# Performance work log

Hardware: AMD Instinct MI355X
Metric: run time of the kernel (lower is better)

Reference implementation:

```python
import jax, jax.numpy as jnp
import numpy as np

NDIR = 6      # build_tree.num_directions()
IDIM = 256
ODIM = 512
B, L, NCH = 8, 4096, 8192


def setup_inputs() -> dict:
    key = jax.random.key(0)
    ks = jax.random.split(key, 9)
    last = jax.random.normal(ks[0], (B, NCH, IDIM), dtype=jnp.float32)
    child_l = jax.random.randint(ks[1], (L,), 0, NCH, dtype=jnp.int32)
    child_r = jax.random.randint(ks[2], (L,), 0, NCH, dtype=jnp.int32)
    vec = jax.random.randint(ks[3], (B, L), 0, NCH, dtype=jnp.int32)
    drev = jax.random.randint(ks[4], (NCH,), 0, 2, dtype=jnp.int32)
    dmap = jax.random.randint(ks[5], (NCH,), 0, NDIR, dtype=jnp.int32)
    # merge FC params: ndir independent Linear(2*idim -> odim) + PReLU(init=relu_weight)
    scale = 1.0 / np.sqrt(2 * IDIM)
    W_merge = jax.random.uniform(ks[6], (NDIR, ODIM, 2 * IDIM), jnp.float32, -scale, scale)
    b_merge = jax.random.uniform(ks[7], (NDIR, ODIM), jnp.float32, -scale, scale)
    alpha_merge = jnp.full((NDIR,), 0.005, dtype=jnp.float32)  # PReLU weight (relu_weight)
    return {"last": last, "W_merge": W_merge, "b_merge": b_merge,
            "alpha_merge": alpha_merge, "child_l": child_l, "child_r": child_r,
            "vec": vec, "drev": drev, "dmap": dmap}


def reference(last, W_merge, b_merge, alpha_merge, child_l, child_r, vec, drev, dmap):
    # child gathers: [B, L, idim]
    lch = last[:, child_l]
    rch = last[:, child_r]
    # per-element direction-reverse blending
    d = drev[vec][:, :, None].astype(last.dtype)          # [B, L, 1]
    a = lch * (1.0 - d) + rch * d
    b = rch * (1.0 - d) + lch * d
    ans = jnp.concatenate([a, b], axis=-1)                # [B, L, 2*idim]
    # routed merge: compute all ndir linears, then select per element (ndir is small)
    y_all = jnp.einsum('bli,doi->bldo', ans, W_merge) + b_merge   # [B, L, ndir, odim]
    dir_idx = dmap[vec]                                   # [B, L] in [0, ndir)
    y = jnp.take_along_axis(y_all, dir_idx[:, :, None, None], axis=2)[:, :, 0]  # [B, L, odim]
    alpha = alpha_merge[dir_idx][:, :, None]              # per-element PReLU slope
    return jnp.where(y > 0, y, alpha * y)
```

## Files before the change

### kernel.cpp

```cpp
#include <hip/hip_runtime.h>
#include <hip/hip_bf16.h>

#define BB 8
#define LL 4096
#define NCH 8192
#define IDIM 256
#define KDIM 512
#define ODIM 512
#define NDIR 6
#define TOT (BB * LL)

typedef short short8 __attribute__((ext_vector_type(8)));
typedef float floatx4 __attribute__((ext_vector_type(4)));

#define IDX_OFF (64 + 2 * TOT)
#define PACKA_OFF_INTS (64 + (2 + NDIR) * TOT)
#define PACKA_ELEMS ((long long)NDIR * TOT * KDIM)
#define W_ELEMS (NDIR * ODIM * KDIM)
#define N_W8 (W_ELEMS / 8)

__device__ inline void async_copy16(const void* g, void* l) {
  __builtin_amdgcn_global_load_lds(
      (const __attribute__((address_space(1))) void*)g,
      (__attribute__((address_space(3))) void*)l, 16, 0, 0);
}

__global__ __launch_bounds__(256) void scatter_kernel(
    const int* __restrict__ vec, const int* __restrict__ child_l,
    const int* __restrict__ child_r, const int* __restrict__ drev,
    const int* __restrict__ dmap, int* __restrict__ ws) {
  __shared__ int lcnt[8];
  __shared__ int gbase[8];
  int tid = threadIdx.x;
  if (tid < 8) lcnt[tid] = 0;
  __syncthreads();

  int lin = blockIdx.x * 256 + tid;
  int l = lin & (LL - 1);
  int v = vec[lin];
  int dir = dmap[v] & 7;
  int sw = drev[v];
  int cl = child_l[l];
  int cr = child_r[l];
  int r0 = sw ? cr : cl;
  int r1 = sw ? cl : cr;
  int pos = atomicAdd(&lcnt[dir], 1);
  __syncthreads();
  if (tid < 8) gbase[tid] = lcnt[tid] ? atomicAdd(&ws[tid], lcnt[tid]) : 0;
  __syncthreads();
  int slot = dir * TOT + gbase[dir] + pos;
  ws[64 + lin] = slot;
  ws[64 + TOT + lin] = r0 | (r1 << 16);
}

__global__ __launch_bounds__(256) void pack_kernel(
    const float* __restrict__ last, const float* __restrict__ W,
    int* __restrict__ ws) {
  __hip_bfloat16* packedA = (__hip_bfloat16*)(ws + PACKA_OFF_INTS);
  __hip_bfloat16* W_bf = packedA + PACKA_ELEMS;
  int bid = blockIdx.x;
  if (bid < TOT / 4) {
    int tid = threadIdx.x;
    int t = bid * 4 + (tid >> 6);
    int L = tid & 63;
    int slot = ws[64 + t];
    int rr = ws[64 + TOT + t];
    int b = t >> 12;
    int r = (L < 32) ? (rr & (NCH - 1)) : ((rr >> 16) & (NCH - 1));
    const floatx4* src =
        (const floatx4*)(last + (long long)(b * NCH + r) * IDIM) + (L & 31) * 2;
    floatx4 x0 = src[0];
    floatx4 x1 = src[1];
    union { short8 v; __hip_bfloat16 h[8]; } u;
    u.h[0] = __float2bfloat16(x0[0]); u.h[1] = __float2bfloat16(x0[1]);
    u.h[2] = __float2bfloat16(x0[2]); u.h[3] = __float2bfloat16(x0[3]);
    u.h[4] = __float2bfloat16(x1[0]); u.h[5] = __float2bfloat16(x1[1]);
    u.h[6] = __float2bfloat16(x1[2]); u.h[7] = __float2bfloat16(x1[3]);
    ((short8*)(packedA + (long long)slot * KDIM + (L >> 5) * IDIM))[L & 31] = u.v;
    if (L == 0) ws[IDX_OFF + slot] = t;
  } else {
    int gid = (bid - TOT / 4) * 256 + threadIdx.x;
    const floatx4* s = (const floatx4*)W;
    floatx4 a = s[2 * gid];
    floatx4 b = s[2 * gid + 1];
    union { short8 v; __hip_bfloat16 h[8]; } u;
    u.h[0] = __float2bfloat16(a[0]); u.h[1] = __float2bfloat16(a[1]);
    u.h[2] = __float2bfloat16(a[2]); u.h[3] = __float2bfloat16(a[3]);
    u.h[4] = __float2bfloat16(b[0]); u.h[5] = __float2bfloat16(b[1]);
    u.h[6] = __float2bfloat16(b[2]); u.h[7] = __float2bfloat16(b[3]);
    ((short8*)W_bf)[gid] = u.v;
  }
}

__global__ __launch_bounds__(256) void gemm_kernel(
    const float* __restrict__ bias, const float* __restrict__ alpha_m,
    const int* __restrict__ ws, float* __restrict__ out) {
  __shared__ __hip_bfloat16 Als[2][128 * 32];
  __shared__ __hip_bfloat16 Bls[2][128 * 32];

  const int mt = blockIdx.y;
  const int nt = blockIdx.x;
  int d = -1, count = 0, m_base = 0;
  {
    int tb = 0;
    for (int dd = 0; dd < NDIR; ++dd) {
      int c = ws[dd];
      int ntile = (c + 127) >> 7;
      if (mt < tb + ntile) { d = dd; count = c; m_base = (mt - tb) * 128; break; }
      tb += ntile;
    }
  }
  if (d < 0) return;

  const __hip_bfloat16* packedA = (const __hip_bfloat16*)(ws + PACKA_OFF_INTS);
  const __hip_bfloat16* W_bf = packedA + PACKA_ELEMS;

  const int tid = threadIdx.x;
  const int wave = __builtin_amdgcn_readfirstlane(tid >> 6);
  const int lane = tid & 63;
  const int lane15 = lane & 15;
  const int quad = lane >> 4;
  const int wm = wave >> 1;
  const int wn = wave & 1;
  const int n_blk = nt * 128;

  const __hip_bfloat16* pa[2];
  const __hip_bfloat16* pb[2];
  int ldsbase[2];
  {
    int f = (lane >> 3) & 3;
    int su = ((lane & 3) ^ f) * 8;
#pragma unroll
    for (int i = 0; i < 2; ++i) {
      int sr = wave * 32 + i * 16 + (lane >> 2);
      ldsbase[i] = (wave * 32 + i * 16) * 32;
      int lr = m_base + sr;
      if (lr >= count) lr = count - 1;
      pa[i] = packedA + (long long)(d * TOT + lr) * KDIM + su;
      pb[i] = W_bf + (long long)(d * ODIM + n_blk + sr) * KDIM + su;
    }
  }

  floatx4 acc[4][4] = {};
  const int xq = (lane15 >> 1) & 3;
  const int xcol = (quad ^ xq) * 8;

#pragma unroll
  for (int i = 0; i < 2; ++i) {
    async_copy16(pa[i], &Als[0][ldsbase[i]]);
    async_copy16(pb[i], &Bls[0][ldsbase[i]]);
  }

#pragma unroll
  for (int kt = 0; kt < 16; ++kt) {
    __syncthreads();
    if (kt < 15) {
      const int nb = (kt + 1) & 1;
      const int ko = (kt + 1) * 32;
#pragma unroll
      for (int i = 0; i < 2; ++i) {
        async_copy16(pa[i] + ko, &Als[nb][ldsbase[i]]);
        async_copy16(pb[i] + ko, &Bls[nb][ldsbase[i]]);
      }
    }
    const int c = kt & 1;
    short8 a[4], b[4];
#pragma unroll
    for (int i = 0; i < 4; ++i)
      a[i] = *(const short8*)&Als[c][(wm * 64 + i * 16 + lane15) * 32 + xcol];
#pragma unroll
    for (int j = 0; j < 4; ++j)
      b[j] = *(const short8*)&Bls[c][(wn * 64 + j * 16 + lane15) * 32 + xcol];
#pragma unroll
    for (int i = 0; i < 4; ++i)
#pragma unroll
      for (int j = 0; j < 4; ++j)
        acc[i][j] = __builtin_amdgcn_mfma_f32_16x16x32_bf16(a[i], b[j], acc[i][j], 0, 0, 0);
  }

  const float alpha = alpha_m[d];
  float bj[4];
#pragma unroll
  for (int j = 0; j < 4; ++j)
    bj[j] = bias[d * ODIM + n_blk + wn * 64 + j * 16 + lane15];

#pragma unroll
  for (int i = 0; i < 4; ++i) {
#pragma unroll
    for (int reg = 0; reg < 4; ++reg) {
      int row_id = m_base + wm * 64 + i * 16 + quad * 4 + reg;
      if (row_id >= count) continue;
      int t = ws[IDX_OFF + d * TOT + row_id] & (TOT - 1);
      float* orow = out + (long long)t * ODIM + n_blk + wn * 64;
#pragma unroll
      for (int j = 0; j < 4; ++j) {
        float y = acc[i][j][reg] + bj[j];
        y = y > 0.f ? y : alpha * y;
        orow[j * 16 + lane15] = y;
      }
    }
  }
}

extern "C" void kernel_launch(void* const* d_in, const int* in_sizes, int n_in,
                              void* d_out, int out_size, void* d_ws, size_t ws_size,
                              hipStream_t stream) {
  const float* last = (const float*)d_in[0];
  const float* W = (const float*)d_in[1];
  const float* bias = (const float*)d_in[2];
  const float* alpha = (const float*)d_in[3];
  const int* child_l = (const int*)d_in[4];
  const int* child_r = (const int*)d_in[5];
  const int* vec = (const int*)d_in[6];
  const int* drev = (const int*)d_in[7];
  const int* dmap = (const int*)d_in[8];

  int* ws = (int*)d_ws;

  hipMemsetAsync(ws, 0, 64 * sizeof(int), stream);
  scatter_kernel<<<TOT / 256, 256, 0, stream>>>(vec, child_l, child_r, drev, dmap, ws);
  pack_kernel<<<TOT / 4 + N_W8 / 256, 256, 0, stream>>>(last, W, ws);
  dim3 grid(ODIM / 128, TOT / 128 + NDIR, 1);
  gemm_kernel<<<grid, 256, 0, stream>>>(bias, alpha, ws, (float*)d_out);
}
```

Before: 176.6 us.

## Gather child rows directly in GEMM instead of materializing packed A

Drops the packed, direction-sorted bf16 A buffer. The prep kernel now converts all of `last` and W to bf16, and the GEMM gathers the two child rows per output row straight from bf16 `last` through per-slot index and row tables written by the scatter kernel. The M tile shrinks from 128 to 64 rows so the launch has more blocks. This avoids writing and re-reading the large packed intermediate, at the cost of converting the whole `last` tensor, including rows that are never used, and of scattered gather loads inside the GEMM.

```diff
diff --git a/kernel.cpp b/kernel.cpp
--- a/kernel.cpp
+++ b/kernel.cpp
@@ -9,20 +9,36 @@
 #define ODIM 512
 #define NDIR 6
 #define TOT (BB * LL)
+#define MT 64
 
 typedef short short8 __attribute__((ext_vector_type(8)));
 typedef float floatx4 __attribute__((ext_vector_type(4)));
 
-#define IDX_OFF (64 + 2 * TOT)
-#define PACKA_OFF_INTS (64 + (2 + NDIR) * TOT)
-#define PACKA_ELEMS ((long long)NDIR * TOT * KDIM)
+#define IDX_OFF 64
+#define ROWS_OFF (64 + NDIR * TOT)
+#define LASTBF_OFF (64 + 2 * NDIR * TOT)
+#define LAST_ELEMS (BB * NCH * IDIM)
 #define W_ELEMS (NDIR * ODIM * KDIM)
+#define N_LAST8 (LAST_ELEMS / 8)
 #define N_W8 (W_ELEMS / 8)
 
 __device__ inline void async_copy16(const void* g, void* l) {
   __builtin_amdgcn_global_load_lds(
       (const __attribute__((address_space(1))) void*)g,
       (__attribute__((address_space(3))) void*)l, 16, 0, 0);
+}
+
+__device__ inline void cvt8(const float* __restrict__ src,
+                            __hip_bfloat16* __restrict__ dst, int i) {
+  const floatx4* s = (const floatx4*)src;
+  floatx4 a = s[2 * i];
+  floatx4 b = s[2 * i + 1];
+  union { short8 v; __hip_bfloat16 h[8]; } u;
+  u.h[0] = __float2bfloat16(a[0]); u.h[1] = __float2bfloat16(a[1]);
+  u.h[2] = __float2bfloat16(a[2]); u.h[3] = __float2bfloat16(a[3]);
+  u.h[4] = __float2bfloat16(b[0]); u.h[5] = __float2bfloat16(b[1]);
+  u.h[6] = __float2bfloat16(b[2]); u.h[7] = __float2bfloat16(b[3]);
+  ((short8*)dst)[i] = u.v;
 }
 
 __global__ __launch_bounds__(256) void scatter_kernel(
@@ -35,9 +51,9 @@
   if (tid < 8) lcnt[tid] = 0;
   __syncthreads();
 
-  int lin = blockIdx.x * 256 + tid;
-  int l = lin & (LL - 1);
-  int v = vec[lin];
+  int t = blockIdx.x * 256 + tid;
+  int l = t & (LL - 1);
+  int v = vec[t];
   int dir = dmap[v] & 7;
   int sw = drev[v];
   int cl = child_l[l];
@@ -49,53 +65,24 @@
   if (tid < 8) gbase[tid] = lcnt[tid] ? atomicAdd(&ws[tid], lcnt[tid]) : 0;
   __syncthreads();
   int slot = dir * TOT + gbase[dir] + pos;
-  ws[64 + lin] = slot;
-  ws[64 + TOT + lin] = r0 | (r1 << 16);
-}
-
-__global__ __launch_bounds__(256) void pack_kernel(
+  ws[IDX_OFF + slot] = t;
+  ws[ROWS_OFF + slot] = r0 | (r1 << 16);
+}
+
+__global__ __launch_bounds__(256) void prep_kernel(
     const float* __restrict__ last, const float* __restrict__ W,
     int* __restrict__ ws) {
-  __hip_bfloat16* packedA = (__hip_bfloat16*)(ws + PACKA_OFF_INTS);
-  __hip_bfloat16* W_bf = packedA + PACKA_ELEMS;
-  int bid = blockIdx.x;
-  if (bid < TOT / 4) {
-    int tid = threadIdx.x;
-    int t = bid * 4 + (tid >> 6);
-    int L = tid & 63;
-    int slot = ws[64 + t];
-    int rr = ws[64 + TOT + t];
-    int b = t >> 12;
-    int r = (L < 32) ? (rr & (NCH - 1)) : ((rr >> 16) & (NCH - 1));
-    const floatx4* src =
-        (const floatx4*)(last + (long long)(b * NCH + r) * IDIM) + (L & 31) * 2;
-    floatx4 x0 = src[0];
-    floatx4 x1 = src[1];
-    union { short8 v; __hip_bfloat16 h[8]; } u;
-    u.h[0] = __float2bfloat16(x0[0]); u.h[1] = __float2bfloat16(x0[1]);
-    u.h[2] = __float2bfloat16(x0[2]); u.h[3] = __float2bfloat16(x0[3]);
-    u.h[4] = __float2bfloat16(x1[0]); u.h[5] = __float2bfloat16(x1[1]);
-    u.h[6] = __float2bfloat16(x1[2]); u.h[7] = __float2bfloat16(x1[3]);
-    ((short8*)(packedA + (long long)slot * KDIM + (L >> 5) * IDIM))[L & 31] = u.v;
-    if (L == 0) ws[IDX_OFF + slot] = t;
-  } else {
-    int gid = (bid - TOT / 4) * 256 + threadIdx.x;
-    const floatx4* s = (const floatx4*)W;
-    floatx4 a = s[2 * gid];
-    floatx4 b = s[2 * gid + 1];
-    union { short8 v; __hip_bfloat16 h[8]; } u;
-    u.h[0] = __float2bfloat16(a[0]); u.h[1] = __float2bfloat16(a[1]);
-    u.h[2] = __float2bfloat16(a[2]); u.h[3] = __float2bfloat16(a[3]);
-    u.h[4] = __float2bfloat16(b[0]); u.h[5] = __float2bfloat16(b[1]);
-    u.h[6] = __float2bfloat16(b[2]); u.h[7] = __float2bfloat16(b[3]);
-    ((short8*)W_bf)[gid] = u.v;
-  }
+  __hip_bfloat16* last_bf = (__hip_bfloat16*)(ws + LASTBF_OFF);
+  __hip_bfloat16* W_bf = last_bf + LAST_ELEMS;
+  int gid = blockIdx.x * 256 + threadIdx.x;
+  if (gid < N_LAST8) cvt8(last, last_bf, gid);
+  else cvt8(W, W_bf, gid - N_LAST8);
 }
 
 __global__ __launch_bounds__(256) void gemm_kernel(
     const float* __restrict__ bias, const float* __restrict__ alpha_m,
     const int* __restrict__ ws, float* __restrict__ out) {
-  __shared__ __hip_bfloat16 Als[2][128 * 32];
+  __shared__ __hip_bfloat16 Als[2][MT * 32];
   __shared__ __hip_bfloat16 Bls[2][128 * 32];
 
   const int mt = blockIdx.y;
@@ -105,15 +92,17 @@
     int tb = 0;
     for (int dd = 0; dd < NDIR; ++dd) {
       int c = ws[dd];
-      int ntile = (c + 127) >> 7;
-      if (mt < tb + ntile) { d = dd; count = c; m_base = (mt - tb) * 128; break; }
+      int ntile = (c + MT - 1) / MT;
+      if (mt < tb + ntile) { d = dd; count = c; m_base = (mt - tb) * MT; break; }
       tb += ntile;
     }
   }
   if (d < 0) return;
 
-  const __hip_bfloat16* packedA = (const __hip_bfloat16*)(ws + PACKA_OFF_INTS);
-  const __hip_bfloat16* W_bf = packedA + PACKA_ELEMS;
+  const __hip_bfloat16* last_bf = (const __hip_bfloat16*)(ws + LASTBF_OFF);
+  const __hip_bfloat16* W_bf = last_bf + LAST_ELEMS;
+  const int* idx = ws + IDX_OFF + d * TOT;
+  const int* rows = ws + ROWS_OFF + d * TOT;
 
   const int tid = threadIdx.x;
   const int wave = __builtin_amdgcn_readfirstlane(tid >> 6);
@@ -124,31 +113,38 @@
   const int wn = wave & 1;
   const int n_blk = nt * 128;
 
-  const __hip_bfloat16* pa[2];
+  const int su = ((tid & 3) ^ ((tid >> 3) & 3)) * 8;
+  const __hip_bfloat16* pa0;
+  const __hip_bfloat16* pa1;
+  {
+    int r = tid >> 2;
+    int lr = m_base + r;
+    if (lr >= count) lr = count - 1;
+    int t = idx[lr] & (TOT - 1);
+    int rr = rows[lr];
+    int b = t >> 12;
+    int r0 = rr & (NCH - 1);
+    int r1 = (rr >> 16) & (NCH - 1);
+    pa0 = last_bf + (long long)(b * NCH + r0) * IDIM + su;
+    pa1 = last_bf + (long long)(b * NCH + r1) * IDIM + su;
+  }
   const __hip_bfloat16* pb[2];
-  int ldsbase[2];
+#pragma unroll
+  for (int i = 0; i < 2; ++i) {
+    int rB = i * 64 + (tid >> 2);
+    pb[i] = W_bf + (long long)(d * ODIM + n_blk + rB) * KDIM + su;
+  }
+  const int aBase = wave * 512;
+  const int bBase0 = wave * 512;
+  const int bBase1 = 2048 + wave * 512;
+
+  floatx4 acc[2][4] = {};
+  const int xcol = (quad ^ ((lane15 >> 1) & 3)) * 8;
+
   {
-    int f = (lane >> 3) & 3;
-    int su = ((lane & 3) ^ f) * 8;
-#pragma unroll
-    for (int i = 0; i < 2; ++i) {
-      int sr = wave * 32 + i * 16 + (lane >> 2);
-      ldsbase[i] = (wave * 32 + i * 16) * 32;
-      int lr = m_base + sr;
-      if (lr >= count) lr = count - 1;
-      pa[i] = packedA + (long long)(d * TOT + lr) * KDIM + su;
-      pb[i] = W_bf + (long long)(d * ODIM + n_blk + sr) * KDIM + su;
-    }
-  }
-
-  floatx4 acc[4][4] = {};
-  const int xq = (lane15 >> 1) & 3;
-  const int xcol = (quad ^ xq) * 8;
-
-#pragma unroll
-  for (int i = 0; i < 2; ++i) {
-    async_copy16(pa[i], &Als[0][ldsbase[i]]);
-    async_copy16(pb[i], &Bls[0][ldsbase[i]]);
+    async_copy16(pa0, &Als[0][aBase]);
+    async_copy16(pb[0], &Bls[0][bBase0]);
+    async_copy16(pb[1], &Bls[0][bBase1]);
   }
 
 #pragma unroll
@@ -156,23 +152,22 @@
     __syncthreads();
     if (kt < 15) {
       const int nb = (kt + 1) & 1;
-      const int ko = (kt + 1) * 32;
-#pragma unroll
-      for (int i = 0; i < 2; ++i) {
-        async_copy16(pa[i] + ko, &Als[nb][ldsbase[i]]);
-        async_copy16(pb[i] + ko, &Bls[nb][ldsbase[i]]);
-      }
+      const int kn = kt + 1;
+      const __hip_bfloat16* ga = (kn < 8) ? pa0 + kn * 32 : pa1 + (kn - 8) * 32;
+      async_copy16(ga, &Als[nb][aBase]);
+      async_copy16(pb[0] + kn * 32, &Bls[nb][bBase0]);
+      async_copy16(pb[1] + kn * 32, &Bls[nb][bBase1]);
     }
     const int c = kt & 1;
-    short8 a[4], b[4];
-#pragma unroll
-    for (int i = 0; i < 4; ++i)
-      a[i] = *(const short8*)&Als[c][(wm * 64 + i * 16 + lane15) * 32 + xcol];
+    short8 a[2], b[4];
+#pragma unroll
+    for (int i = 0; i < 2; ++i)
+      a[i] = *(const short8*)&Als[c][(wm * 32 + i * 16 + lane15) * 32 + xcol];
 #pragma unroll
     for (int j = 0; j < 4; ++j)
       b[j] = *(const short8*)&Bls[c][(wn * 64 + j * 16 + lane15) * 32 + xcol];
 #pragma unroll
-    for (int i = 0; i < 4; ++i)
+    for (int i = 0; i < 2; ++i)
 #pragma unroll
       for (int j = 0; j < 4; ++j)
         acc[i][j] = __builtin_amdgcn_mfma_f32_16x16x32_bf16(a[i], b[j], acc[i][j], 0, 0, 0);
@@ -185,12 +180,12 @@
     bj[j] = bias[d * ODIM + n_blk + wn * 64 + j * 16 + lane15];
 
 #pragma unroll
-  for (int i = 0; i < 4; ++i) {
+  for (int i = 0; i < 2; ++i) {
 #pragma unroll
     for (int reg = 0; reg < 4; ++reg) {
-      int row_id = m_base + wm * 64 + i * 16 + quad * 4 + reg;
+      int row_id = m_base + wm * 32 + i * 16 + quad * 4 + reg;
       if (row_id >= count) continue;
-      int t = ws[IDX_OFF + d * TOT + row_id] & (TOT - 1);
+      int t = idx[row_id] & (TOT - 1);
       float* orow = out + (long long)t * ODIM + n_blk + wn * 64;
 #pragma unroll
       for (int j = 0; j < 4; ++j) {
@@ -217,9 +212,9 @@
 
   int* ws = (int*)d_ws;
 
-  hipMemsetAsync(ws, 0, 64 * sizeof(int), stream);
+  hipMemsetAsync(ws, 0, 32, stream);
   scatter_kernel<<<TOT / 256, 256, 0, stream>>>(vec, child_l, child_r, drev, dmap, ws);
-  pack_kernel<<<TOT / 4 + N_W8 / 256, 256, 0, stream>>>(last, W, ws);
-  dim3 grid(ODIM / 128, TOT / 128 + NDIR, 1);
+  prep_kernel<<<(N_LAST8 + N_W8) / 256, 256, 0, stream>>>(last, W, ws);
+  dim3 grid(ODIM / 128, TOT / MT + NDIR, 1);
   gemm_kernel<<<grid, 256, 0, stream>>>(bias, alpha, ws, (float*)d_out);
 }
```

Measured after the change: 173.5 us. Within noise of the previous version (-1.8%).
